# Performance work log

Hardware: AMD Instinct MI355X
Metric: run time of the kernel (lower is better)

Reference implementation:

```python
import jax, jax.numpy as jnp
import numpy as np

N_NODES = 20000
N_EDGES = 640000
NUM_FEATURES = 128
HIDDEN = 64
HEADS = 4
NUM_CLASSES = 16
NEG_SLOPE = 0.2  # PyG GATConv default leaky_relu slope


def gat_conv(x, src, dst, W, att_s, att_d, b, num_nodes, concat):
    """PyG-style GATConv (inference: attention dropout is identity).
    x: [N, F_in]; src/dst: [E] (self-loops already included);
    W: [F_in, H*C]; att_s/att_d: [H, C]; b: [H*C] or [C]."""
    H, C = att_s.shape
    h = (x @ W).reshape(num_nodes, H, C)            # [N,H,C]
    a_s = jnp.sum(h * att_s, axis=-1)               # [N,H]
    a_d = jnp.sum(h * att_d, axis=-1)               # [N,H]
    e = jax.nn.leaky_relu(a_s[src] + a_d[dst], NEG_SLOPE)  # [E,H]
    # softmax over incoming edges of each destination node
    emax = jax.ops.segment_max(e, dst, num_segments=num_nodes)  # [N,H]
    ex = jnp.exp(e - emax[dst])
    denom = jax.ops.segment_sum(ex, dst, num_segments=num_nodes)
    alpha = ex / denom[dst]                         # [E,H]
    msg = h[src] * alpha[..., None]                 # [E,H,C]
    out = jax.ops.segment_sum(msg, dst, num_segments=num_nodes)  # [N,H,C]
    out = out.reshape(num_nodes, H * C) if concat else out.mean(axis=1)
    return out + b


def setup_inputs() -> dict:
    key = jax.random.key(0)
    ks = jax.random.split(key, 12)
    d1_in, d1_out = NUM_FEATURES, HEADS * HIDDEN
    d2_in, d2_out = HEADS * HIDDEN, HEADS * HIDDEN
    return {
        "x": jax.random.normal(ks[0], (N_NODES, NUM_FEATURES), dtype=jnp.float32),
        "edge_index": jax.random.randint(ks[1], (2, N_EDGES), 0, N_NODES, dtype=jnp.int64)
        if jax.config.jax_enable_x64 else
        jax.random.randint(ks[1], (2, N_EDGES), 0, N_NODES, dtype=jnp.int32),
        "W1": jax.random.normal(ks[2], (d1_in, d1_out), dtype=jnp.float32) / np.sqrt(d1_in),
        "att_src1": jax.random.normal(ks[3], (HEADS, HIDDEN), dtype=jnp.float32) / np.sqrt(HIDDEN),
        "att_dst1": jax.random.normal(ks[4], (HEADS, HIDDEN), dtype=jnp.float32) / np.sqrt(HIDDEN),
        "b1": jnp.zeros((HEADS * HIDDEN,), dtype=jnp.float32),
        "W2": jax.random.normal(ks[5], (d2_in, d2_out), dtype=jnp.float32) / np.sqrt(d2_in),
        "att_src2": jax.random.normal(ks[6], (HEADS, HIDDEN), dtype=jnp.float32) / np.sqrt(HIDDEN),
        "att_dst2": jax.random.normal(ks[7], (HEADS, HIDDEN), dtype=jnp.float32) / np.sqrt(HIDDEN),
        "b2": jnp.zeros((HIDDEN,), dtype=jnp.float32),
        "Wout": jax.random.normal(ks[8], (HIDDEN, NUM_CLASSES), dtype=jnp.float32) / np.sqrt(HIDDEN),
        "bout": jnp.zeros((NUM_CLASSES,), dtype=jnp.float32),
    }


def reference(x, edge_index, W1, att_src1, att_dst1, b1, W2, att_src2, att_dst2, b2, Wout, bout):
    N = x.shape[0]
    loops = jnp.arange(N, dtype=edge_index.dtype)
    src = jnp.concatenate([edge_index[0], loops])   # PyG add_self_loops=True
    dst = jnp.concatenate([edge_index[1], loops])
    h = gat_conv(x, src, dst, W1, att_src1, att_dst1, b1, N, concat=True)
    h = jax.nn.elu(h)                               # dropout is identity at eval
    h = gat_conv(h, src, dst, W2, att_src2, att_dst2, b2, N, concat=False)
    return h @ Wout + bout
```

## Files before the change

### kernel.cpp

```cpp
#include <hip/hip_runtime.h>
#include <hip/hip_bf16.h>
#include <hip/hip_fp16.h>


#define HEADS 4
#define CDIM 64
#define HC 256

typedef __attribute__((ext_vector_type(8))) short bf16x8;
typedef __attribute__((ext_vector_type(4))) float f32x4;

__device__ __forceinline__ short f32_to_bf16_rne(float v) {
  unsigned u = __float_as_uint(v);
  unsigned r = (u + 0x7FFFu + ((u >> 16) & 1u)) >> 16;
  return (short)r;
}
__device__ __forceinline__ float bf16_bits_to_f32(short s) {
  return __uint_as_float(((unsigned)(unsigned short)s) << 16);
}

__global__ __launch_bounds__(256) void pack_w_kernel(
    const float* __restrict__ W, short* __restrict__ Wt_hi,
    short* __restrict__ Wt_lo, int K, int total) {
  const int i = blockIdx.x * 256 + threadIdx.x;
  if (i >= total) return;
  const int k = i >> 8, n = i & 255;
  const float v = W[i];
  const short hi = f32_to_bf16_rne(v);
  const short lo = f32_to_bf16_rne(v - bf16_bits_to_f32(hi));
  Wt_hi[(size_t)n * K + k] = hi;
  Wt_lo[(size_t)n * K + k] = lo;
}

__global__ __launch_bounds__(128) void gemm_mfma_split(
    const float* __restrict__ A, const short* __restrict__ Wt_hi,
    const short* __restrict__ Wt_lo, __half* __restrict__ h16,
    const float* __restrict__ att_s, const float* __restrict__ att_d,
    float* __restrict__ a_s, float* __restrict__ a_d, int M, int K) {
  __shared__ alignas(16) short As_hi[64 * 32];
  __shared__ alignas(16) short As_lo[64 * 32];
  const int t = threadIdx.x;
  const int wave = t >> 6;
  const int lane = t & 63;
  const int quad = lane >> 4;
  const int m16 = lane & 15;
  const int row0 = blockIdx.x * 64;
  const int col0 = blockIdx.y * 128 + wave * 64;
  const int head = col0 >> 6;

  f32x4 acc[4][4] = {};

  for (int k0 = 0; k0 < K; k0 += 32) {
    if (k0) __syncthreads();
#pragma unroll
    for (int uu = 0; uu < 2; ++uu) {
      const int u = t + uu * 128;
      const int r = u >> 2, seg = u & 3;
      const int gr = row0 + r;
      float vv[8] = {0.f, 0.f, 0.f, 0.f, 0.f, 0.f, 0.f, 0.f};
      if (gr < M) {
        const float* ap = A + (size_t)gr * K + k0 + seg * 8;
        const float4 v0 = *(const float4*)ap;
        const float4 v1 = *(const float4*)(ap + 4);
        vv[0] = v0.x; vv[1] = v0.y; vv[2] = v0.z; vv[3] = v0.w;
        vv[4] = v1.x; vv[5] = v1.y; vv[6] = v1.z; vv[7] = v1.w;
      }
      bf16x8 h8, l8;
#pragma unroll
      for (int j = 0; j < 8; ++j) {
        const short hi = f32_to_bf16_rne(vv[j]);
        h8[j] = hi;
        l8[j] = f32_to_bf16_rne(vv[j] - bf16_bits_to_f32(hi));
      }
      *(bf16x8*)(As_hi + r * 32 + seg * 8) = h8;
      *(bf16x8*)(As_lo + r * 32 + seg * 8) = l8;
    }
    bf16x8 b_hi[4], b_lo[4];
#pragma unroll
    for (int nt = 0; nt < 4; ++nt) {
      const size_t off = (size_t)(col0 + nt * 16 + m16) * K + k0 + quad * 8;
      b_hi[nt] = *(const bf16x8*)(Wt_hi + off);
      b_lo[nt] = *(const bf16x8*)(Wt_lo + off);
    }
    __syncthreads();
    bf16x8 a_hi[4], a_lo[4];
#pragma unroll
    for (int mt = 0; mt < 4; ++mt) {
      const int off = (mt * 16 + m16) * 32 + quad * 8;
      a_hi[mt] = *(const bf16x8*)(As_hi + off);
      a_lo[mt] = *(const bf16x8*)(As_lo + off);
    }
#pragma unroll
    for (int mt = 0; mt < 4; ++mt)
#pragma unroll
      for (int nt = 0; nt < 4; ++nt) {
        acc[mt][nt] = __builtin_amdgcn_mfma_f32_16x16x32_bf16(
            a_hi[mt], b_hi[nt], acc[mt][nt], 0, 0, 0);
        acc[mt][nt] = __builtin_amdgcn_mfma_f32_16x16x32_bf16(
            a_hi[mt], b_lo[nt], acc[mt][nt], 0, 0, 0);
        acc[mt][nt] = __builtin_amdgcn_mfma_f32_16x16x32_bf16(
            a_lo[mt], b_hi[nt], acc[mt][nt], 0, 0, 0);
      }
  }
  float sa[4], da[4];
#pragma unroll
  for (int nt = 0; nt < 4; ++nt) {
    sa[nt] = att_s[col0 + nt * 16 + m16];
    da[nt] = att_d[col0 + nt * 16 + m16];
  }
#pragma unroll
  for (int mt = 0; mt < 4; ++mt)
#pragma unroll
    for (int r = 0; r < 4; ++r) {
      const int gr = row0 + mt * 16 + quad * 4 + r;
      float ps = acc[mt][0][r] * sa[0] + acc[mt][1][r] * sa[1] +
                 acc[mt][2][r] * sa[2] + acc[mt][3][r] * sa[3];
      float pd = acc[mt][0][r] * da[0] + acc[mt][1][r] * da[1] +
                 acc[mt][2][r] * da[2] + acc[mt][3][r] * da[3];
#pragma unroll
      for (int off = 1; off <= 8; off <<= 1) {
        ps += __shfl_xor(ps, off);
        pd += __shfl_xor(pd, off);
      }
      if (gr < M) {
        if (m16 == 0) {
          a_s[gr * HEADS + head] = ps;
          a_d[gr * HEADS + head] = pd;
        }
#pragma unroll
        for (int nt = 0; nt < 4; ++nt)
          h16[(size_t)gr * HC + col0 + nt * 16 + m16] =
              __float2half(acc[mt][nt][r]);
      }
    }
}

__global__ __launch_bounds__(256) void deg_count_kernel(
    const int* __restrict__ dst, int* __restrict__ deg, int E_raw, int Etot) {
  const int e = blockIdx.x * 256 + threadIdx.x;
  if (e >= Etot) return;
  const int d = (e < E_raw) ? dst[e] : (e - E_raw);
  atomicAdd(&deg[d], 1);
}

__global__ __launch_bounds__(256) void scan_block_kernel(
    const int* __restrict__ deg, int* __restrict__ incl,
    int* __restrict__ bsum, int N) {
  __shared__ int sm[256];
  const int t = threadIdx.x;
  const int i = blockIdx.x * 256 + t;
  int v = (i < N) ? deg[i] : 0;
  sm[t] = v;
  __syncthreads();
#pragma unroll
  for (int off = 1; off < 256; off <<= 1) {
    int x = (t >= off) ? sm[t - off] : 0;
    __syncthreads();
    sm[t] += x;
    __syncthreads();
  }
  if (i < N) incl[i] = sm[t];
  if (t == 255) bsum[blockIdx.x] = sm[255];
}

__global__ __launch_bounds__(256) void scan_top_kernel(
    const int* __restrict__ bsum, int* __restrict__ boff, int nb) {
  __shared__ int sm[256];
  const int t = threadIdx.x;
  int v = (t < nb) ? bsum[t] : 0;
  sm[t] = v;
  __syncthreads();
#pragma unroll
  for (int off = 1; off < 256; off <<= 1) {
    int x = (t >= off) ? sm[t - off] : 0;
    __syncthreads();
    sm[t] += x;
    __syncthreads();
  }
  if (t < nb) boff[t] = sm[t] - v;
}

__global__ __launch_bounds__(256) void scan_final_kernel(
    const int* __restrict__ deg, const int* __restrict__ incl,
    const int* __restrict__ boff, int* __restrict__ row_ptr,
    int* __restrict__ cursor, int N, int Etot) {
  const int i = blockIdx.x * 256 + threadIdx.x;
  if (i == 0) row_ptr[N] = Etot;
  if (i >= N) return;
  const int v = boff[blockIdx.x] + incl[i] - deg[i];
  row_ptr[i] = v;
  cursor[i] = v;
}

__global__ __launch_bounds__(256) void csr_scatter_kernel(
    const int* __restrict__ src, const int* __restrict__ dst,
    int* __restrict__ cursor, int* __restrict__ csr_src, int E_raw, int Etot) {
  const int e = blockIdx.x * 256 + threadIdx.x;
  if (e >= Etot) return;
  const int s = (e < E_raw) ? src[e] : (e - E_raw);
  const int d = (e < E_raw) ? dst[e] : (e - E_raw);
  const int pos = atomicAdd(&cursor[d], 1);
  csr_src[pos] = s;
}

__device__ __forceinline__ void acc_edge_f16(float ex, const uint4& u,
                                             float4& A, float4& B) {
  const __half2* hp = (const __half2*)&u;
  float2 f;
  f = __half22float2(hp[0]); A.x += ex * f.x; A.y += ex * f.y;
  f = __half22float2(hp[1]); A.z += ex * f.x; A.w += ex * f.y;
  f = __half22float2(hp[2]); B.x += ex * f.x; B.y += ex * f.y;
  f = __half22float2(hp[3]); B.z += ex * f.x; B.w += ex * f.y;
}

__global__ __launch_bounds__(256) void gat_aggregate_kernel(
    const int* __restrict__ row_ptr, const int* __restrict__ csr_src,
    const __half* __restrict__ h16, const float* __restrict__ a_s,
    const float* __restrict__ a_d, const float* __restrict__ b,
    float* __restrict__ out, int mode) {
  const int bid = blockIdx.x;
  const int hd = bid & 3;
  const int n = (bid >> 2) * 4 + (threadIdx.x >> 6);
  const int lane = threadIdx.x & 63;
  const int q = lane >> 3;
  const int oc = lane & 7;
  const float ad = a_d[n * HEADS + hd];
  const int beg = row_ptr[n];
  const int end = row_ptr[n + 1];
  const char* hbase = (const char*)h16 + hd * 128 + oc * 16;
  const float* asb = a_s + hd;
  float4 accA = {0.f, 0.f, 0.f, 0.f}, accB = {0.f, 0.f, 0.f, 0.f};
  float den = 0.f;
  int i = beg + q;
  for (; i + 8 < end; i += 16) {
    const int s0 = csr_src[i];
    const int s1 = csr_src[i + 8];
    const float as0 = asb[s0 * 4];
    const float as1 = asb[s1 * 4];
    const uint4 u0 = *(const uint4*)(hbase + ((unsigned)s0 << 9));
    const uint4 u1 = *(const uint4*)(hbase + ((unsigned)s1 << 9));
    float a0 = as0 + ad; a0 = (a0 > 0.f) ? a0 : 0.2f * a0;
    float a1 = as1 + ad; a1 = (a1 > 0.f) ? a1 : 0.2f * a1;
    const float e0 = __expf(a0);
    const float e1 = __expf(a1);
    den += e0 + e1;
    acc_edge_f16(e0, u0, accA, accB);
    acc_edge_f16(e1, u1, accA, accB);
  }
  for (; i < end; i += 8) {
    const int s = csr_src[i];
    float a = asb[s * 4] + ad;
    a = (a > 0.f) ? a : 0.2f * a;
    const float ex = __expf(a);
    den += ex;
    const uint4 u = *(const uint4*)(hbase + ((unsigned)s << 9));
    acc_edge_f16(ex, u, accA, accB);
  }
#pragma unroll
  for (int off = 8; off <= 32; off <<= 1) {
    accA.x += __shfl_xor(accA.x, off);
    accA.y += __shfl_xor(accA.y, off);
    accA.z += __shfl_xor(accA.z, off);
    accA.w += __shfl_xor(accA.w, off);
    accB.x += __shfl_xor(accB.x, off);
    accB.y += __shfl_xor(accB.y, off);
    accB.z += __shfl_xor(accB.z, off);
    accB.w += __shfl_xor(accB.w, off);
    den    += __shfl_xor(den, off);
  }
  if (lane < 8) {
    const float inv = 1.f / den;
    float u[8] = {accA.x * inv, accA.y * inv, accA.z * inv, accA.w * inv,
                  accB.x * inv, accB.y * inv, accB.z * inv, accB.w * inv};
    if (mode == 0) {
      const int cb = hd * CDIM + oc * 8;
#pragma unroll
      for (int k = 0; k < 8; ++k) {
        const float t = u[k] + b[cb + k];
        u[k] = (t > 0.f) ? t : (__expf(t) - 1.f);
      }
    }
    float* op = out + (size_t)n * HC + hd * CDIM + oc * 8;
    *(float4*)op = make_float4(u[0], u[1], u[2], u[3]);
    *(float4*)(op + 4) = make_float4(u[4], u[5], u[6], u[7]);
  }
}

__global__ __launch_bounds__(256) void final_fused_kernel(
    const float* __restrict__ agg, const float* __restrict__ b2,
    const float* __restrict__ Wout, const float* __restrict__ bout,
    float* __restrict__ out, int N) {
  const int n = blockIdx.x * 4 + (threadIdx.x >> 6);
  const int c = threadIdx.x & 63;
  if (n >= N) return;
  const float* ar = agg + (size_t)n * HC;
  const float m = 0.25f * (ar[c] + ar[c + 64] + ar[c + 128] + ar[c + 192]) +
                  b2[c];
  const float4* wr = (const float4*)(Wout + c * 16);
  const float4 w0 = wr[0], w1 = wr[1], w2 = wr[2], w3 = wr[3];
  float p[16] = {m * w0.x, m * w0.y, m * w0.z, m * w0.w,
                 m * w1.x, m * w1.y, m * w1.z, m * w1.w,
                 m * w2.x, m * w2.y, m * w2.z, m * w2.w,
                 m * w3.x, m * w3.y, m * w3.z, m * w3.w};
#pragma unroll
  for (int off = 1; off < 64; off <<= 1)
#pragma unroll
    for (int j = 0; j < 16; ++j) p[j] += __shfl_xor(p[j], off);
  if (c == 0) {
    float* op = out + (size_t)n * 16;
    *(float4*)op = make_float4(p[0] + bout[0], p[1] + bout[1],
                               p[2] + bout[2], p[3] + bout[3]);
    *(float4*)(op + 4) = make_float4(p[4] + bout[4], p[5] + bout[5],
                                     p[6] + bout[6], p[7] + bout[7]);
    *(float4*)(op + 8) = make_float4(p[8] + bout[8], p[9] + bout[9],
                                     p[10] + bout[10], p[11] + bout[11]);
    *(float4*)(op + 12) = make_float4(p[12] + bout[12], p[13] + bout[13],
                                      p[14] + bout[14], p[15] + bout[15]);
  }
}

extern "C" void kernel_launch(void* const* d_in, const int* in_sizes, int n_in,
                              void* d_out, int out_size, void* d_ws, size_t ws_size,
                              hipStream_t stream) {
  const float* x      = (const float*)d_in[0];
  const int*   eidx   = (const int*)d_in[1];
  const float* W1     = (const float*)d_in[2];
  const float* att_s1 = (const float*)d_in[3];
  const float* att_d1 = (const float*)d_in[4];
  const float* b1     = (const float*)d_in[5];
  const float* W2     = (const float*)d_in[6];
  const float* att_s2 = (const float*)d_in[7];
  const float* att_d2 = (const float*)d_in[8];
  const float* b2     = (const float*)d_in[9];
  const float* Wout   = (const float*)d_in[10];
  const float* bout   = (const float*)d_in[11];
  float* out          = (float*)d_out;

  const int N     = in_sizes[0] / 128;
  const int E_raw = in_sizes[1] / 2;
  const int Etot  = E_raw + N;
  const int* src = eidx;
  const int* dst = eidx + E_raw;
  const int NB = (N + 255) / 256;

  float* ws = (float*)d_ws;
  float* buf_agg = ws;
  float* buf_as  = buf_agg + (size_t)N * HC;
  float* buf_ad  = buf_as + (size_t)N * HEADS;
  __half* h16    = (__half*)(buf_ad + (size_t)N * HEADS);
  int* deg     = (int*)(h16 + (size_t)N * HC);
  int* incl    = deg + N;
  int* row_ptr = incl + N;
  int* cursor  = row_ptr + (N + 1);
  int* bsum    = cursor + N;
  int* boff    = bsum + NB;
  int* csr_src = boff + NB;
  uintptr_t wp = ((uintptr_t)(csr_src + Etot) + 15) & ~(uintptr_t)15;
  short* wt1_hi = (short*)wp;
  short* wt1_lo = wt1_hi + 256 * 128;
  short* wt2_hi = wt1_lo + 256 * 128;
  short* wt2_lo = wt2_hi + 256 * 256;

  const dim3 blk(256);
  const int g_edge = (Etot + 255) / 256;
  const dim3 g_gemm((N + 63) / 64, 2);
  const dim3 blk_gemm(128);

  pack_w_kernel<<<(128 * 256 + 255) / 256, blk, 0, stream>>>(W1, wt1_hi, wt1_lo,
                                                             128, 128 * 256);
  pack_w_kernel<<<(256 * 256 + 255) / 256, blk, 0, stream>>>(W2, wt2_hi, wt2_lo,
                                                             256, 256 * 256);
  hipMemsetAsync(deg, 0, (size_t)N * sizeof(int), stream);
  deg_count_kernel<<<g_edge, blk, 0, stream>>>(dst, deg, E_raw, Etot);
  scan_block_kernel<<<NB, blk, 0, stream>>>(deg, incl, bsum, N);
  scan_top_kernel<<<1, blk, 0, stream>>>(bsum, boff, NB);
  scan_final_kernel<<<NB, blk, 0, stream>>>(deg, incl, boff, row_ptr, cursor, N, Etot);
  csr_scatter_kernel<<<g_edge, blk, 0, stream>>>(src, dst, cursor, csr_src, E_raw, Etot);

  gemm_mfma_split<<<g_gemm, blk_gemm, 0, stream>>>(
      x, wt1_hi, wt1_lo, h16, att_s1, att_d1, buf_as, buf_ad, N, 128);
  gat_aggregate_kernel<<<N, blk, 0, stream>>>(row_ptr, csr_src, h16, buf_as,
                                              buf_ad, b1, buf_agg, 0);

  gemm_mfma_split<<<g_gemm, blk_gemm, 0, stream>>>(
      buf_agg, wt2_hi, wt2_lo, h16, att_s2, att_d2, buf_as, buf_ad, N, 256);
  gat_aggregate_kernel<<<N, blk, 0, stream>>>(row_ptr, csr_src, h16, buf_as,
                                              buf_ad, b2, buf_agg, 1);

  final_fused_kernel<<<(N + 3) / 4, blk, 0, stream>>>(buf_agg, b2, Wout, bout,
                                                      out, N);
}
```

Measured before the change: 310.1 us.

## Remap aggregation lanes to 16 edges x 4 channel groups and use fdot2 accumulation

The per-head aggregation kernel now assigns each lane 16 channels (two 16-byte loads) across 4 channel groups, so 16 edges are in flight per wave instead of 8. Each edge pair's two exp weights are packed into half2 and accumulated with v_dot2 (fdot2) after perm-interleaving the two rows, which halves the FMA count. The shuffle reduction gains one extra level and the accumulator register count doubles. The exp weights are rounded to fp16 via pkrtz, which lowers accumulation precision and could overflow if the un-max-subtracted exps exceed the half range.

Result: slower. 350.5 us (+13.0%).

```diff
diff --git a/kernel.cpp b/kernel.cpp
--- a/kernel.cpp
+++ b/kernel.cpp
@@ -9,6 +9,15 @@
 
 typedef __attribute__((ext_vector_type(8))) short bf16x8;
 typedef __attribute__((ext_vector_type(4))) float f32x4;
+typedef _Float16 __attribute__((ext_vector_type(2))) f16x2;
+
+#if __has_builtin(__builtin_amdgcn_fdot2) && \
+    __has_builtin(__builtin_amdgcn_cvt_pkrtz) && \
+    __has_builtin(__builtin_amdgcn_perm)
+#define USE_FDOT2 1
+#else
+#define USE_FDOT2 0
+#endif
 
 __device__ __forceinline__ short f32_to_bf16_rne(float v) {
   unsigned u = __float_as_uint(v);
@@ -203,14 +212,22 @@
   csr_src[pos] = s;
 }
 
-__device__ __forceinline__ void acc_edge_f16(float ex, const uint4& u,
-                                             float4& A, float4& B) {
-  const __half2* hp = (const __half2*)&u;
-  float2 f;
-  f = __half22float2(hp[0]); A.x += ex * f.x; A.y += ex * f.y;
-  f = __half22float2(hp[1]); A.z += ex * f.x; A.w += ex * f.y;
-  f = __half22float2(hp[2]); B.x += ex * f.x; B.y += ex * f.y;
-  f = __half22float2(hp[3]); B.z += ex * f.x; B.w += ex * f.y;
+__device__ __forceinline__ void fma16_f16(float ex, const uint4& A,
+                                          const uint4& B, float* acc) {
+  const __half2* hp0 = (const __half2*)&A;
+  const __half2* hp1 = (const __half2*)&B;
+#pragma unroll
+  for (int j = 0; j < 4; ++j) {
+    float2 f = __half22float2(hp0[j]);
+    acc[2 * j] += ex * f.x;
+    acc[2 * j + 1] += ex * f.y;
+  }
+#pragma unroll
+  for (int j = 0; j < 4; ++j) {
+    float2 f = __half22float2(hp1[j]);
+    acc[8 + 2 * j] += ex * f.x;
+    acc[8 + 2 * j + 1] += ex * f.y;
+  }
 }
 
 __global__ __launch_bounds__(256) void gat_aggregate_kernel(
@@ -222,67 +239,96 @@
   const int hd = bid & 3;
   const int n = (bid >> 2) * 4 + (threadIdx.x >> 6);
   const int lane = threadIdx.x & 63;
-  const int q = lane >> 3;
-  const int oc = lane & 7;
+  const int es = lane >> 2;
+  const int cs = lane & 3;
   const float ad = a_d[n * HEADS + hd];
   const int beg = row_ptr[n];
   const int end = row_ptr[n + 1];
-  const char* hbase = (const char*)h16 + hd * 128 + oc * 16;
+  const char* hb = (const char*)h16 + hd * 128;
+  const unsigned csoff = (unsigned)cs << 5;
   const float* asb = a_s + hd;
-  float4 accA = {0.f, 0.f, 0.f, 0.f}, accB = {0.f, 0.f, 0.f, 0.f};
+  float acc[16];
+#pragma unroll
+  for (int k = 0; k < 16; ++k) acc[k] = 0.f;
   float den = 0.f;
-  int i = beg + q;
-  for (; i + 8 < end; i += 16) {
+  int i = beg + es;
+  for (; i + 16 < end; i += 32) {
     const int s0 = csr_src[i];
-    const int s1 = csr_src[i + 8];
+    const int s1 = csr_src[i + 16];
     const float as0 = asb[s0 * 4];
     const float as1 = asb[s1 * 4];
-    const uint4 u0 = *(const uint4*)(hbase + ((unsigned)s0 << 9));
-    const uint4 u1 = *(const uint4*)(hbase + ((unsigned)s1 << 9));
-    float a0 = as0 + ad; a0 = (a0 > 0.f) ? a0 : 0.2f * a0;
-    float a1 = as1 + ad; a1 = (a1 > 0.f) ? a1 : 0.2f * a1;
-    const float e0 = __expf(a0);
-    const float e1 = __expf(a1);
+    const unsigned off0 = ((unsigned)s0 << 9) + csoff;
+    const unsigned off1 = ((unsigned)s1 << 9) + csoff;
+    const uint4 ua0 = *(const uint4*)(hb + off0);
+    const uint4 ua1 = *(const uint4*)(hb + off0 + 16);
+    const uint4 ub0 = *(const uint4*)(hb + off1);
+    const uint4 ub1 = *(const uint4*)(hb + off1 + 16);
+    float t0 = as0 + ad; t0 = fmaxf(t0, 0.2f * t0);
+    float t1 = as1 + ad; t1 = fmaxf(t1, 0.2f * t1);
+    const float e0 = __expf(t0);
+    const float e1 = __expf(t1);
     den += e0 + e1;
-    acc_edge_f16(e0, u0, accA, accB);
-    acc_edge_f16(e1, u1, accA, accB);
-  }
-  for (; i < end; i += 8) {
+#if USE_FDOT2
+    const f16x2 exh = __builtin_bit_cast(
+        f16x2, __builtin_amdgcn_cvt_pkrtz(e0, e1));
+#define DOT2STEP(u0r, u1r, k)                                                 \
+    {                                                                         \
+      const unsigned lo_ = __builtin_amdgcn_perm(u1r, u0r, 0x05040100u);      \
+      const unsigned hi_ = __builtin_amdgcn_perm(u1r, u0r, 0x07060302u);      \
+      acc[k] = __builtin_amdgcn_fdot2(exh, __builtin_bit_cast(f16x2, lo_),    \
+                                      acc[k], false);                         \
+      acc[k + 1] = __builtin_amdgcn_fdot2(                                    \
+          exh, __builtin_bit_cast(f16x2, hi_), acc[k + 1], false);            \
+    }
+    DOT2STEP(ua0.x, ub0.x, 0)
+    DOT2STEP(ua0.y, ub0.y, 2)
+    DOT2STEP(ua0.z, ub0.z, 4)
+    DOT2STEP(ua0.w, ub0.w, 6)
+    DOT2STEP(ua1.x, ub1.x, 8)
+    DOT2STEP(ua1.y, ub1.y, 10)
+    DOT2STEP(ua1.z, ub1.z, 12)
+    DOT2STEP(ua1.w, ub1.w, 14)
+#undef DOT2STEP
+#else
+    fma16_f16(e0, ua0, ua1, acc);
+    fma16_f16(e1, ub0, ub1, acc);
+#endif
+  }
+  for (; i < end; i += 16) {
     const int s = csr_src[i];
-    float a = asb[s * 4] + ad;
-    a = (a > 0.f) ? a : 0.2f * a;
-    const float ex = __expf(a);
+    float t0 = asb[s * 4] + ad;
+    t0 = fmaxf(t0, 0.2f * t0);
+    const float ex = __expf(t0);
     den += ex;
-    const uint4 u = *(const uint4*)(hbase + ((unsigned)s << 9));
-    acc_edge_f16(ex, u, accA, accB);
-  }
-#pragma unroll
-  for (int off = 8; off <= 32; off <<= 1) {
-    accA.x += __shfl_xor(accA.x, off);
-    accA.y += __shfl_xor(accA.y, off);
-    accA.z += __shfl_xor(accA.z, off);
-    accA.w += __shfl_xor(accA.w, off);
-    accB.x += __shfl_xor(accB.x, off);
-    accB.y += __shfl_xor(accB.y, off);
-    accB.z += __shfl_xor(accB.z, off);
-    accB.w += __shfl_xor(accB.w, off);
-    den    += __shfl_xor(den, off);
-  }
-  if (lane < 8) {
+    const unsigned off = ((unsigned)s << 9) + csoff;
+    const uint4 u0 = *(const uint4*)(hb + off);
+    const uint4 u1 = *(const uint4*)(hb + off + 16);
+    fma16_f16(ex, u0, u1, acc);
+  }
+#pragma unroll
+  for (int off = 4; off <= 32; off <<= 1) {
+#pragma unroll
+    for (int k = 0; k < 16; ++k) acc[k] += __shfl_xor(acc[k], off);
+    den += __shfl_xor(den, off);
+  }
+  if (lane < 4) {
     const float inv = 1.f / den;
-    float u[8] = {accA.x * inv, accA.y * inv, accA.z * inv, accA.w * inv,
-                  accB.x * inv, accB.y * inv, accB.z * inv, accB.w * inv};
+    float u[16];
+#pragma unroll
+    for (int k = 0; k < 16; ++k) u[k] = acc[k] * inv;
     if (mode == 0) {
-      const int cb = hd * CDIM + oc * 8;
-#pragma unroll
-      for (int k = 0; k < 8; ++k) {
-        const float t = u[k] + b[cb + k];
-        u[k] = (t > 0.f) ? t : (__expf(t) - 1.f);
-      }
-    }
-    float* op = out + (size_t)n * HC + hd * CDIM + oc * 8;
-    *(float4*)op = make_float4(u[0], u[1], u[2], u[3]);
-    *(float4*)(op + 4) = make_float4(u[4], u[5], u[6], u[7]);
+      const float* bb = b + hd * CDIM + cs * 16;
+#pragma unroll
+      for (int k = 0; k < 16; ++k) {
+        const float t0 = u[k] + bb[k];
+        u[k] = (t0 > 0.f) ? t0 : (__expf(t0) - 1.f);
+      }
+    }
+    float* op = out + (size_t)n * HC + hd * CDIM + cs * 16;
+#pragma unroll
+    for (int k = 0; k < 4; ++k)
+      *(float4*)(op + 4 * k) =
+          make_float4(u[4 * k], u[4 * k + 1], u[4 * k + 2], u[4 * k + 3]);
   }
 }
 
```
